# Kernel tuning notes

Measured on AMD Instinct MI355X. Metric: run time of the kernel, lower is better.

The kernel has to match this reference:

```python
import jax, jax.numpy as jnp
import numpy as np

KINEMATIC_CHAIN = [[0,2,5,8,11],[0,1,4,7,10],[0,3,6,9,12,15],[9,14,17,19,21],[9,13,16,18,20]]
_paths = [c[1:] for c in KINEMATIC_CHAIN]
SEG_S = np.array([p[i] for p in _paths for i in range(len(p)-1)])      # [16] segment start joints
SEG_E = np.array([p[i+1] for p in _paths for i in range(len(p)-1)])    # [16] segment end joints
PATH_ID = np.array([k for k, p in enumerate(_paths) for _ in range(len(p)-1)])
N_PATHS = len(_paths)
P_ONEHOT = (PATH_ID[:, None] == np.arange(N_PATHS)[None, :]).astype(np.float32)  # [16,5]


def _safe_normalize(v):
    ss = jnp.sum(v * v, axis=-1, keepdims=True)
    return jnp.where(ss > 0, v / jnp.sqrt(jnp.where(ss > 0, ss, 1.0)), 0.0)


def _gli_pairwise(s1, e1, s2, e2):
    # all inputs broadcast to [..., 3]; returns Gauss linking integral per segment pair
    r13, r14 = s2 - s1, e2 - s1
    r23, r24 = s2 - e1, e2 - e1
    r12, r34 = e1 - s1, e2 - s2
    f0 = _safe_normalize(jnp.cross(r13, r14))
    f1 = _safe_normalize(jnp.cross(r14, r24))
    f2 = _safe_normalize(jnp.cross(r24, r23))
    f3 = _safe_normalize(jnp.cross(r23, r13))
    def asin_dot(a, b):
        return jnp.arcsin(jnp.clip(jnp.sum(a * b, -1), -1.0, 1.0))
    total = asin_dot(f0, f1) + asin_dot(f1, f2) + asin_dot(f2, f3) + asin_dot(f3, f0)
    sign = jnp.sum(jnp.cross(r34, r12) * r13, -1)
    mult = jnp.where(sign <= 0, -1.0, 1.0)
    return mult * total / (4.0 * jnp.pi)


def _bbox_xz(m):
    x, z = m[..., 0], m[..., 2]
    return x.min(-1), x.max(-1), z.min(-1), z.max(-1)


def setup_inputs() -> dict:
    key = jax.random.key(0)
    k1, k2 = jax.random.split(key)
    B, F, J = 64, 240, 22
    motion1 = jax.random.normal(k1, (B, F, J, 3), dtype=jnp.float32)
    motion2 = jax.random.normal(k2, (B, F, J, 3), dtype=jnp.float32)
    return {"motion1": motion1, "motion2": motion2}


def reference(motion1, motion2):
    B, F = motion1.shape[0], motion1.shape[1]
    P = jnp.asarray(P_ONEHOT, motion1.dtype)
    # gather all 16 skeleton segments, broadcast to 16x16 segment pairs
    s1 = motion1[..., SEG_S, :][..., :, None, :]   # [B,F,16,1,3]
    e1 = motion1[..., SEG_E, :][..., :, None, :]
    s2 = motion2[..., SEG_S, :][..., None, :, :]   # [B,F,1,16,3]
    e2 = motion2[..., SEG_E, :][..., None, :, :]
    gli_seg = _gli_pairwise(s1, e1, s2, e2)        # [B,F,16,16]
    # sum segment-pair GLIs into path-pair blocks -> [B,F,5,5]
    gli_pose = jnp.einsum('bfmn,mi,nj->bfij', gli_seg, P, P)

    # xz bounding-box overlap per frame, then dilate by 1 frame (window start-1..end+1)
    nx1, xx1, nz1, xz1 = _bbox_xz(motion1)
    nx2, xx2, nz2, xz2 = _bbox_xz(motion2)
    flag = (xx1 >= nx2) & (xx2 >= nx1) & (xz1 >= nz2) & (xz2 >= nz1)   # [B,F]
    pad = jnp.zeros_like(flag[:, :1])
    mask = flag | jnp.concatenate([flag[:, 1:], pad], 1) | jnp.concatenate([pad, flag[:, :-1]], 1)
    gli_motion = gli_pose * mask[..., None, None].astype(gli_pose.dtype)

    vel = jnp.abs(gli_motion[:, 1:] - gli_motion[:, :-1]).reshape(B, F - 1, -1)
    return vel.max(-1)
```

## Files before the change

kernel.cpp:

```cpp
#include <hip/hip_runtime.h>
#include <math.h>

#define BB 64
#define FF 240
#define NJ 22
#define NFRM (BB * FF)

#define PK8(a0,a1,a2,a3,a4,a5,a6,a7) \
  (  (unsigned long long)(a0)        | ((unsigned long long)(a1) << 5)  \
   | ((unsigned long long)(a2) << 10)| ((unsigned long long)(a3) << 15) \
   | ((unsigned long long)(a4) << 20)| ((unsigned long long)(a5) << 25) \
   | ((unsigned long long)(a6) << 30)| ((unsigned long long)(a7) << 35) )
static constexpr unsigned long long SEG_S_LO = PK8(2,5,8,1,4,7,3,6);
static constexpr unsigned long long SEG_S_HI = PK8(9,12,14,17,19,13,16,18);
static constexpr unsigned long long SEG_E_LO = PK8(5,8,11,4,7,10,6,9);
static constexpr unsigned long long SEG_E_HI = PK8(12,15,17,19,21,16,18,20);
static constexpr unsigned PO_PK = 0u | (3u<<5) | (6u<<10) | (10u<<15) | (13u<<20);
static constexpr unsigned PC_PK = 3u | (3u<<5) | (4u<<10) | (3u<<15)  | (3u<<20);

struct F3 { float x, y, z; };
__device__ __forceinline__ F3 sub(F3 a, F3 b){ return {a.x-b.x, a.y-b.y, a.z-b.z}; }
__device__ __forceinline__ F3 crs(F3 a, F3 b){
    return {fmaf(a.y, b.z, -a.z*b.y), fmaf(a.z, b.x, -a.x*b.z), fmaf(a.x, b.y, -a.y*b.x)};
}
__device__ __forceinline__ float dt(F3 a, F3 b){ return fmaf(a.x, b.x, fmaf(a.y, b.y, a.z*b.z)); }
__device__ __forceinline__ float clamp1(float d){ return fminf(fmaxf(d, -1.0f), 1.0f); }

__device__ __forceinline__ float asin_fast(float d){
    float ax = fabsf(d);
    float p = fmaf(fmaf(fmaf(-0.0187293f, ax, 0.0742610f), ax, -0.2121144f), ax, 1.5707288f);
    float r = 1.57079632679f - __builtin_amdgcn_sqrtf(1.0f - ax) * p;
    return copysignf(r, d);
}

__global__ void __launch_bounds__(128, 8) k_main(const float* __restrict__ m1,
                                                 const float* __restrict__ m2,
                                                 float* __restrict__ gp,
                                                 int* __restrict__ flags){
    __shared__ __align__(16) float pts[2][2][68];
    __shared__ __align__(16) float seg[2][2][16][12];
    __shared__ float g[2][256];
    __shared__ float ext[2][8];
    int tid = threadIdx.x;
    int w = tid >> 6, lane = tid & 63;
    int fr = blockIdx.x * 2 + w;

    const float2* gsrc1 = (const float2*)(m1 + (size_t)fr * 66);
    const float2* gsrc2 = (const float2*)(m2 + (size_t)fr * 66);
    if (lane < 33) ((float2*)pts[w][0])[lane] = gsrc1[lane];
    if (lane >= 31){ int u = lane - 31; if (u < 33) ((float2*)pts[w][1])[u] = gsrc2[u]; }
    __syncthreads();

    if (lane < 32){
        int m = lane & 15, mot = lane >> 4;
        unsigned long long ps = (m < 8) ? SEG_S_LO : SEG_S_HI;
        unsigned long long pe = (m < 8) ? SEG_E_LO : SEG_E_HI;
        int sh = (m & 7) * 5;
        int js = (int)((ps >> sh) & 31);
        int je = (int)((pe >> sh) & 31);
        const float* P = pts[w][mot];
        float* d = &seg[w][mot][m][0];
        d[0] = P[js*3]; d[1] = P[js*3+1]; d[2] = P[js*3+2];
        d[3] = P[je*3]; d[4] = P[je*3+1]; d[5] = P[je*3+2];
    } else if (lane < 40){
        int sel = lane - 32;
        int mot = sel >> 2;
        int c = sel & 2;
        bool mx = sel & 1;
        const float* P = pts[w][mot];
        float a = 1e30f;
        #pragma unroll
        for (int j = 0; j < NJ; ++j){
            float v = P[j*3 + c];
            a = fminf(a, mx ? -v : v);
        }
        ext[w][sel] = mx ? -a : a;
    }
    __syncthreads();

    int n = lane & 15, q = lane >> 4;
    float4 sa = *(const float4*)&seg[w][1][n][0];
    float2 sb = *(const float2*)&seg[w][1][n][4];
    F3 s2 = {sa.x, sa.y, sa.z};
    F3 e2 = {sa.w, sb.x, sb.y};

    float rd01[4], rd12[4], rd23[4], rd30[4];
    float q01[4], q12[4], q23[4], q30[4];
    float sg[4];
    #pragma unroll
    for (int k = 0; k < 4; ++k){
        int m = q + 4 * k;
        float4 ta = *(const float4*)&seg[w][0][m][0];
        float2 tb = *(const float2*)&seg[w][0][m][4];
        F3 s1 = {ta.x, ta.y, ta.z};
        F3 e1 = {ta.w, tb.x, tb.y};
        F3 r13 = sub(s2, s1), r14 = sub(e2, s1);
        F3 r23 = sub(s2, e1), r24 = sub(e2, e1);
        F3 f0 = crs(r13, r14);
        F3 f1 = crs(r14, r24);
        F3 f2 = crs(r24, r23);
        F3 f3 = crs(r23, r13);
        float ss0 = dt(f0,f0), ss1 = dt(f1,f1), ss2 = dt(f2,f2), ss3 = dt(f3,f3);
        rd01[k] = dt(f0,f1); rd12[k] = dt(f1,f2);
        rd23[k] = dt(f2,f3); rd30[k] = dt(f3,f0);
        q01[k] = ss0*ss1; q12[k] = ss1*ss2; q23[k] = ss2*ss3; q30[k] = ss3*ss0;
        sg[k] = dt(f3, r14);
    }
    float i01[4], i12[4], i23[4], i30[4];
    #pragma unroll
    for (int k = 0; k < 4; ++k){
        i01[k] = rsqrtf(fmaxf(q01[k], 1e-30f));
        i12[k] = rsqrtf(fmaxf(q12[k], 1e-30f));
        i23[k] = rsqrtf(fmaxf(q23[k], 1e-30f));
        i30[k] = rsqrtf(fmaxf(q30[k], 1e-30f));
    }
    #pragma unroll
    for (int k = 0; k < 4; ++k){
        float t = asin_fast(clamp1(rd01[k] * i01[k]))
                + asin_fast(clamp1(rd12[k] * i12[k]))
                + asin_fast(clamp1(rd23[k] * i23[k]))
                + asin_fast(clamp1(rd30[k] * i30[k]));
        float r = (sg[k] >= 0.0f ? -t : t) * 0.07957747154594767f;
        g[w][(k << 6) | lane] = r;
    }
    __syncthreads();

    if (lane < 25){
        int i = lane / 5, j = lane - i * 5;
        int poi = (int)((PO_PK >> (i*5)) & 31), pci = (int)((PC_PK >> (i*5)) & 31);
        int poj = (int)((PO_PK >> (j*5)) & 31), pcj = (int)((PC_PK >> (j*5)) & 31);
        float s = 0.0f;
        for (int a = 0; a < pci; ++a)
            for (int b = 0; b < pcj; ++b)
                s += g[w][(poi + a) * 16 + (poj + b)];
        int bb = fr / FF, f = fr - bb * FF;
        gp[((size_t)bb * 25 + lane) * FF + f] = s;
    } else if (lane == 25){
        flags[fr] = (ext[w][1] >= ext[w][4] && ext[w][5] >= ext[w][0] &&
                     ext[w][3] >= ext[w][6] && ext[w][7] >= ext[w][2]) ? 1 : 0;
    }
}

__global__ void __launch_bounds__(256) k_vel(const float* __restrict__ gp,
                                             const int* __restrict__ flags,
                                             float* __restrict__ out){
    int b = blockIdx.x;
    int f = threadIdx.x;
    if (f >= FF - 1) return;
    const int* fl = flags + b * FF;

    int v0 = fl[f] | fl[f + 1];
    if (f > 0) v0 |= fl[f - 1];
    float mk0 = v0 ? 1.0f : 0.0f;

    int v1 = fl[f] | fl[f + 1];
    if (f + 2 < FF) v1 |= fl[f + 2];
    float mk1 = v1 ? 1.0f : 0.0f;

    const float* gb = gp + (size_t)b * 25 * FF + f;
    float mx = 0.0f;
    #pragma unroll
    for (int p = 0; p < 25; ++p){
        float g0 = gb[p * FF];
        float g1 = gb[p * FF + 1];
        float d = fabsf(g1 * mk1 - g0 * mk0);
        mx = fmaxf(mx, d);
    }
    out[b * (FF - 1) + f] = mx;
}

extern "C" void kernel_launch(void* const* d_in, const int* in_sizes, int n_in,
                              void* d_out, int out_size, void* d_ws, size_t ws_size,
                              hipStream_t stream) {
    const float* m1 = (const float*)d_in[0];
    const float* m2 = (const float*)d_in[1];
    float* gp    = (float*)d_ws;
    int*   flags = (int*)((char*)d_ws + (size_t)BB * 25 * FF * 4);
    float* out = (float*)d_out;

    k_main<<<NFRM / 2, 128, 0, stream>>>(m1, m2, gp, flags);
    k_vel<<<BB, 256, 0, stream>>>(gp, flags, out);
}
```

Measured before the change: 81.76 us.

## Process two frames per wavefront and four wavefronts per block in k_main

```diff
diff --git a/kernel.cpp b/kernel.cpp
--- a/kernel.cpp
+++ b/kernel.cpp
@@ -33,111 +33,136 @@
     return copysignf(r, d);
 }
 
-__global__ void __launch_bounds__(128, 8) k_main(const float* __restrict__ m1,
+__global__ void __launch_bounds__(256, 4) k_main(const float* __restrict__ m1,
                                                  const float* __restrict__ m2,
                                                  float* __restrict__ gp,
                                                  int* __restrict__ flags){
-    __shared__ __align__(16) float pts[2][2][68];
-    __shared__ __align__(16) float seg[2][2][16][12];
-    __shared__ float g[2][256];
-    __shared__ float ext[2][8];
+    __shared__ __align__(16) float pts[4][2][136];
+    __shared__ __align__(8)  float seg[4][2][2][16][6];
+    __shared__ float g[4][2][256];
+    __shared__ float ext[4][2][8];
     int tid = threadIdx.x;
     int w = tid >> 6, lane = tid & 63;
-    int fr = blockIdx.x * 2 + w;
-
-    const float2* gsrc1 = (const float2*)(m1 + (size_t)fr * 66);
-    const float2* gsrc2 = (const float2*)(m2 + (size_t)fr * 66);
-    if (lane < 33) ((float2*)pts[w][0])[lane] = gsrc1[lane];
-    if (lane >= 31){ int u = lane - 31; if (u < 33) ((float2*)pts[w][1])[u] = gsrc2[u]; }
+    int fr0 = blockIdx.x * 8 + w * 2;
+
+    const float2* gs1 = (const float2*)(m1 + (size_t)fr0 * 66);
+    const float2* gs2 = (const float2*)(m2 + (size_t)fr0 * 66);
+    for (int u = lane; u < 132; u += 64){
+        bool a = u < 66;
+        int v = a ? u : u - 66;
+        ((float2*)pts[w][a ? 0 : 1])[v] = (a ? gs1 : gs2)[v];
+    }
     __syncthreads();
 
-    if (lane < 32){
-        int m = lane & 15, mot = lane >> 4;
+    {
+        int m = lane & 15, mot = (lane >> 4) & 1, f = lane >> 5;
         unsigned long long ps = (m < 8) ? SEG_S_LO : SEG_S_HI;
         unsigned long long pe = (m < 8) ? SEG_E_LO : SEG_E_HI;
         int sh = (m & 7) * 5;
         int js = (int)((ps >> sh) & 31);
         int je = (int)((pe >> sh) & 31);
-        const float* P = pts[w][mot];
-        float* d = &seg[w][mot][m][0];
+        const float* P = &pts[w][mot][f * 66];
+        float* d = &seg[w][f][mot][m][0];
         d[0] = P[js*3]; d[1] = P[js*3+1]; d[2] = P[js*3+2];
         d[3] = P[je*3]; d[4] = P[je*3+1]; d[5] = P[je*3+2];
-    } else if (lane < 40){
-        int sel = lane - 32;
-        int mot = sel >> 2;
-        int c = sel & 2;
-        bool mx = sel & 1;
-        const float* P = pts[w][mot];
+    }
+    if (lane < 16){
+        int f = lane >> 3, mot = (lane >> 2) & 1;
+        int c = lane & 2;
+        bool mx = lane & 1;
+        const float* P = &pts[w][mot][f * 66];
         float a = 1e30f;
         #pragma unroll
         for (int j = 0; j < NJ; ++j){
             float v = P[j*3 + c];
             a = fminf(a, mx ? -v : v);
         }
-        ext[w][sel] = mx ? -a : a;
+        ext[w][f][lane & 7] = mx ? -a : a;
     }
     __syncthreads();
 
     int n = lane & 15, q = lane >> 4;
-    float4 sa = *(const float4*)&seg[w][1][n][0];
-    float2 sb = *(const float2*)&seg[w][1][n][4];
-    F3 s2 = {sa.x, sa.y, sa.z};
-    F3 e2 = {sa.w, sb.x, sb.y};
-
-    float rd01[4], rd12[4], rd23[4], rd30[4];
-    float q01[4], q12[4], q23[4], q30[4];
-    float sg[4];
+    F3 s2f[2], e2f[2];
+    #pragma unroll
+    for (int f = 0; f < 2; ++f){
+        const float* B = &seg[w][f][1][n][0];
+        float2 b0 = *(const float2*)(B+0);
+        float2 b1 = *(const float2*)(B+2);
+        float2 b2 = *(const float2*)(B+4);
+        s2f[f] = {b0.x, b0.y, b1.x};
+        e2f[f] = {b1.y, b2.x, b2.y};
+    }
+
+    float rd01[2][4], rd12[2][4], rd23[2][4], rd30[2][4];
+    float q01[2][4], q12[2][4], q23[2][4], q30[2][4];
+    float sg[2][4];
+    #pragma unroll
+    for (int f = 0; f < 2; ++f){
+        F3 s2 = s2f[f], e2 = e2f[f];
+        #pragma unroll
+        for (int k = 0; k < 4; ++k){
+            int m = q + 4 * k;
+            const float* A = &seg[w][f][0][m][0];
+            float2 a0 = *(const float2*)(A+0);
+            float2 a1 = *(const float2*)(A+2);
+            float2 a2 = *(const float2*)(A+4);
+            F3 s1 = {a0.x, a0.y, a1.x};
+            F3 e1 = {a1.y, a2.x, a2.y};
+            F3 r13 = sub(s2, s1), r14 = sub(e2, s1);
+            F3 r23 = sub(s2, e1), r24 = sub(e2, e1);
+            F3 f0 = crs(r13, r14);
+            F3 f1 = crs(r14, r24);
+            F3 f2 = crs(r24, r23);
+            F3 f3 = crs(r23, r13);
+            float ss0 = dt(f0,f0), ss1 = dt(f1,f1), ss2 = dt(f2,f2), ss3 = dt(f3,f3);
+            rd01[f][k] = dt(f0,f1); rd12[f][k] = dt(f1,f2);
+            rd23[f][k] = dt(f2,f3); rd30[f][k] = dt(f3,f0);
+            q01[f][k] = ss0*ss1; q12[f][k] = ss1*ss2;
+            q23[f][k] = ss2*ss3; q30[f][k] = ss3*ss0;
+            sg[f][k] = dt(f3, r14);
+        }
+    }
+    float i01[2][4], i12[2][4], i23[2][4], i30[2][4];
+    #pragma unroll
+    for (int f = 0; f < 2; ++f)
     #pragma unroll
     for (int k = 0; k < 4; ++k){
-        int m = q + 4 * k;
-        float4 ta = *(const float4*)&seg[w][0][m][0];
-        float2 tb = *(const float2*)&seg[w][0][m][4];
-        F3 s1 = {ta.x, ta.y, ta.z};
-        F3 e1 = {ta.w, tb.x, tb.y};
-        F3 r13 = sub(s2, s1), r14 = sub(e2, s1);
-        F3 r23 = sub(s2, e1), r24 = sub(e2, e1);
-        F3 f0 = crs(r13, r14);
-        F3 f1 = crs(r14, r24);
-        F3 f2 = crs(r24, r23);
-        F3 f3 = crs(r23, r13);
-        float ss0 = dt(f0,f0), ss1 = dt(f1,f1), ss2 = dt(f2,f2), ss3 = dt(f3,f3);
-        rd01[k] = dt(f0,f1); rd12[k] = dt(f1,f2);
-        rd23[k] = dt(f2,f3); rd30[k] = dt(f3,f0);
-        q01[k] = ss0*ss1; q12[k] = ss1*ss2; q23[k] = ss2*ss3; q30[k] = ss3*ss0;
-        sg[k] = dt(f3, r14);
-    }
-    float i01[4], i12[4], i23[4], i30[4];
+        i01[f][k] = rsqrtf(fmaxf(q01[f][k], 1e-30f));
+        i12[f][k] = rsqrtf(fmaxf(q12[f][k], 1e-30f));
+        i23[f][k] = rsqrtf(fmaxf(q23[f][k], 1e-30f));
+        i30[f][k] = rsqrtf(fmaxf(q30[f][k], 1e-30f));
+    }
+    #pragma unroll
+    for (int f = 0; f < 2; ++f)
     #pragma unroll
     for (int k = 0; k < 4; ++k){
-        i01[k] = rsqrtf(fmaxf(q01[k], 1e-30f));
-        i12[k] = rsqrtf(fmaxf(q12[k], 1e-30f));
-        i23[k] = rsqrtf(fmaxf(q23[k], 1e-30f));
-        i30[k] = rsqrtf(fmaxf(q30[k], 1e-30f));
-    }
-    #pragma unroll
-    for (int k = 0; k < 4; ++k){
-        float t = asin_fast(clamp1(rd01[k] * i01[k]))
-                + asin_fast(clamp1(rd12[k] * i12[k]))
-                + asin_fast(clamp1(rd23[k] * i23[k]))
-                + asin_fast(clamp1(rd30[k] * i30[k]));
-        float r = (sg[k] >= 0.0f ? -t : t) * 0.07957747154594767f;
-        g[w][(k << 6) | lane] = r;
+        float t = asin_fast(clamp1(rd01[f][k] * i01[f][k]))
+                + asin_fast(clamp1(rd12[f][k] * i12[f][k]))
+                + asin_fast(clamp1(rd23[f][k] * i23[f][k]))
+                + asin_fast(clamp1(rd30[f][k] * i30[f][k]));
+        float r = (sg[f][k] >= 0.0f ? -t : t) * 0.07957747154594767f;
+        g[w][f][(k << 6) | lane] = r;
     }
     __syncthreads();
 
-    if (lane < 25){
-        int i = lane / 5, j = lane - i * 5;
+    if (lane < 50){
+        int f = lane >= 25 ? 1 : 0;
+        int pp = lane - f * 25;
+        int i = pp / 5, j = pp - i * 5;
         int poi = (int)((PO_PK >> (i*5)) & 31), pci = (int)((PC_PK >> (i*5)) & 31);
         int poj = (int)((PO_PK >> (j*5)) & 31), pcj = (int)((PC_PK >> (j*5)) & 31);
         float s = 0.0f;
         for (int a = 0; a < pci; ++a)
             for (int b = 0; b < pcj; ++b)
-                s += g[w][(poi + a) * 16 + (poj + b)];
-        int bb = fr / FF, f = fr - bb * FF;
-        gp[((size_t)bb * 25 + lane) * FF + f] = s;
-    } else if (lane == 25){
-        flags[fr] = (ext[w][1] >= ext[w][4] && ext[w][5] >= ext[w][0] &&
-                     ext[w][3] >= ext[w][6] && ext[w][7] >= ext[w][2]) ? 1 : 0;
+                s += g[w][f][(poi + a) * 16 + (poj + b)];
+        int fr = fr0 + f;
+        int bb = fr / FF, ff = fr - bb * FF;
+        gp[((size_t)bb * 25 + pp) * FF + ff] = s;
+    } else if (lane < 52){
+        int f = lane - 50;
+        const float* e = ext[w][f];
+        flags[fr0 + f] = (e[1] >= e[4] && e[5] >= e[0] &&
+                          e[3] >= e[6] && e[7] >= e[2]) ? 1 : 0;
     }
 }
 
@@ -178,6 +203,6 @@
     int*   flags = (int*)((char*)d_ws + (size_t)BB * 25 * FF * 4);
     float* out = (float*)d_out;
 
-    k_main<<<NFRM / 2, 128, 0, stream>>>(m1, m2, gp, flags);
+    k_main<<<NFRM / 8, 256, 0, stream>>>(m1, m2, gp, flags);
     k_vel<<<BB, 256, 0, stream>>>(gp, flags, out);
 }
```

After: 78.22 us. -4.3%, faster.
